# Kernel optimization log

Measured on AMD Instinct MI355X. Metric: run time of the kernel, lower is better.

Reference implementation:

```python
import jax, jax.numpy as jnp
import numpy as np

B, N, DIM = 1, 512, 1024
HEADS, DH = 16, 64          # dim_head = 64, _dim = heads*dh = 1024
P = 32                      # projection_dim
P2 = P // 2
NEG_INF = -1e30


def setup_inputs() -> dict:
    key = jax.random.key(0)
    ks = jax.random.split(key, 14)
    s = 0.02
    _dim = HEADS * DH
    return {
        "x":    jax.random.normal(ks[0], (B, N, DIM), dtype=jnp.float32),
        "Wqkv": jax.random.normal(ks[1], (3 * _dim, DIM), dtype=jnp.float32) * s,
        "Wout": jax.random.normal(ks[2], (DIM, _dim), dtype=jnp.float32) * s,
        "Wq":   jax.random.normal(ks[3], (P, DH), dtype=jnp.float32) * s,
        "bq":   jax.random.normal(ks[4], (P,), dtype=jnp.float32) * s,
        "Wk":   jax.random.normal(ks[5], (P, DH), dtype=jnp.float32) * s,
        "bk":   jax.random.normal(ks[6], (P,), dtype=jnp.float32) * s,
        "W1":   jax.random.normal(ks[7], (P, 2 * P), dtype=jnp.float32) * s,
        "b1":   jax.random.normal(ks[8], (P,), dtype=jnp.float32) * s,
        "W2":   jax.random.normal(ks[9], (P2, P), dtype=jnp.float32) * s,
        "b2":   jax.random.normal(ks[10], (P2,), dtype=jnp.float32) * s,
        "W3":   jax.random.normal(ks[11], (1, P2), dtype=jnp.float32) * s,
        "b3":   jax.random.normal(ks[12], (1,), dtype=jnp.float32) * s,
    }


def reference(x, Wqkv, Wout, Wq, bq, Wk, bk, W1, b1, W2, b2, W3, b3):
    b, n, _ = x.shape
    # qkv projection, then einops 'b n (d k h) -> k b h n d' split (d outermost!)
    qkv = jnp.einsum('bnc,oc->bno', x, Wqkv).reshape(b, n, DH, 3, HEADS)
    q = jnp.transpose(qkv[:, :, :, 0, :], (0, 3, 1, 2))  # [b,h,n,dh]
    k = jnp.transpose(qkv[:, :, :, 1, :], (0, 3, 1, 2))
    v = jnp.transpose(qkv[:, :, :, 2, :], (0, 3, 1, 2))

    qp = jnp.einsum('bhnd,pd->bhnp', q, Wq) + bq  # [b,h,n,P]
    kp = jnp.einsum('bhnd,pd->bhnp', k, Wk) + bk

    # linear1 on concat(q_i, k_j): split W1 -> broadcast-add (same math,
    # avoids materializing the [b,h,n,n,2P] concat tensor)
    W1q, W1k = W1[:, :P], W1[:, P:]
    a = jnp.einsum('bhnp,qp->bhnq', qp, W1q)      # [b,h,n,P]
    c = jnp.einsum('bhnp,qp->bhnq', kp, W1k)      # [b,h,n,P]
    h1 = jax.nn.relu(a[:, :, :, None, :] + c[:, :, None, :, :] + b1)  # [b,h,n,n,P]
    h2 = jax.nn.relu(jnp.einsum('bhijp,qp->bhijq', h1, W2) + b2)      # [b,h,n,n,P/2]
    score = jnp.einsum('bhijq,oq->bhijo', h2, W3)[..., 0] + b3[0]     # [b,h,n,n]

    # causal mask (triu(1) filled with -inf)
    i = jnp.arange(n)
    causal = i[None, :] > i[:, None]
    score = jnp.where(causal, NEG_INF, score)

    attn = jax.nn.softmax(score, axis=-1)
    out = jnp.einsum('bhij,bhjd->bhid', attn, v)                      # [b,h,n,dh]
    out = jnp.transpose(out, (0, 2, 1, 3)).reshape(b, n, HEADS * DH)  # b n (h d)
    return jnp.einsum('bne,oe->bno', out, Wout)
```

## Files before the change

### kernel.cpp

```cpp
#include <hip/hip_runtime.h>
#include <hip/hip_bf16.h>
#include <hip/hip_fp16.h>
#include <math.h>

#define N_SEQ 512
#define DIM   1024
#define HEADS 16
#define DH    64
#define P     32
#define P2    16
#define PSTR  520

typedef short    bf16x8 __attribute__((ext_vector_type(8)));
typedef _Float16 f16x8  __attribute__((ext_vector_type(8)));
typedef float    f32x4  __attribute__((ext_vector_type(4)));

__device__ inline unsigned short f2bf(float f) {
  union { float f; unsigned u; } v; v.f = f;
  unsigned r = (v.u + 0x7fffu + ((v.u >> 16) & 1u)) >> 16;
  return (unsigned short)r;
}

union H8 { f16x8 v; __half2 h2[4]; unsigned u32[4]; };

__global__ __launch_bounds__(256) void prep(
    const float* __restrict__ Wqkv, const float* __restrict__ Wq,
    const float* __restrict__ bq, const float* __restrict__ Wk,
    const float* __restrict__ bk, const float* __restrict__ W1,
    const float* __restrict__ x, const float* __restrict__ Wout,
    short* __restrict__ Wcomb, short* __restrict__ xb,
    short* __restrict__ Woutb, float* __restrict__ ba32,
    float* __restrict__ bc32) {
  const int b = blockIdx.x, tid = threadIdx.x;
  if (b < 256) {
    __shared__ float W1s[32][33];
    __shared__ float Wqs[32][65];
    __shared__ float wsm[32][65];
    __shared__ __align__(16) float qs[64][132];
    const int part = b >> 7, rem = b & 127;
    const int h = rem >> 3, c0 = (rem & 7) * 128;
    const int grow = part * 16 + h;
    for (int idx = tid; idx < 1024; idx += 256)
      W1s[idx >> 5][idx & 31] = W1[(idx >> 5) * 64 + part * 32 + (idx & 31)];
    const float* Wsel = part ? Wk : Wq;
    for (int idx = tid; idx < 2048; idx += 256)
      Wqs[idx >> 6][idx & 63] = Wsel[idx];
    for (int idx = tid; idx < 2048; idx += 256) {
      const int d = idx >> 5, c4 = idx & 31;
      *(float4*)&qs[d][c4 * 4] =
          *(const float4*)(Wqkv + (size_t)(d * 48 + grow) * DIM + c0 + c4 * 4);
    }
    __syncthreads();
    for (int idx = tid; idx < 2048; idx += 256) {
      const int q = idx >> 6, d = idx & 63;
      float s = 0.f;
#pragma unroll
      for (int p = 0; p < 32; ++p) s += W1s[q][p] * Wqs[p][d];
      wsm[q][d] = s;
    }
    __syncthreads();
    for (int idx = tid; idx < 4096; idx += 256) {
      const int q = idx >> 7, c = idx & 127;
      float s = 0.f;
#pragma unroll
      for (int d = 0; d < 64; ++d) s += wsm[q][d] * qs[d][c];
      Wcomb[(size_t)(part * 512 + h * 32 + q) * DIM + c0 + c] = (short)f2bf(s);
    }
    if (rem == 0 && tid < 32) {
      const float* bsel = part ? bk : bq;
      float s = 0.f;
#pragma unroll
      for (int p = 0; p < 32; ++p) s += W1s[tid][p] * bsel[p];
      (part ? bc32 : ba32)[tid] = s;
    }
  } else if (b < 384) {
#pragma unroll
    for (int rr = 0; rr < 8; ++rr) {
      const int ov = (b - 256) * 8 + rr;
      const int h = ov >> 6, d = ov & 63;
      const float4 v = *(const float4*)(Wqkv + (size_t)(d * 48 + 32 + h) * DIM + tid * 4);
      ushort4 o;
      o.x = f2bf(v.x); o.y = f2bf(v.y); o.z = f2bf(v.z); o.w = f2bf(v.w);
      *(ushort4*)(Wcomb + (size_t)(1024 + ov) * DIM + tid * 4) = o;
    }
  } else if (b < 512) {
    const int idx = (b - 384) * 256 + tid;
#pragma unroll
    for (int u = 0; u < 4; ++u) {
      const int t = u * 32768 + idx;
      const float4 v = ((const float4*)x)[t];
      ushort4 o;
      o.x = f2bf(v.x); o.y = f2bf(v.y); o.z = f2bf(v.z); o.w = f2bf(v.w);
      ((ushort4*)xb)[t] = o;
    }
  } else {
    const int idx = (b - 512) * 256 + tid;
#pragma unroll
    for (int u = 0; u < 4; ++u) {
      const int t = u * 65536 + idx;
      const float4 v = ((const float4*)Wout)[t];
      ushort4 o;
      o.x = f2bf(v.x); o.y = f2bf(v.y); o.z = f2bf(v.z); o.w = f2bf(v.w);
      ((ushort4*)Woutb)[t] = o;
    }
  }
}

__global__ __launch_bounds__(256) void gemm_acv(
    const short* __restrict__ xb, const short* __restrict__ Wcomb,
    const float* __restrict__ ba32, const float* __restrict__ bc32,
    const float* __restrict__ b1,
    __half* __restrict__ a_buf, __half* __restrict__ cb_buf,
    __half* __restrict__ vT) {
  const int wave = blockIdx.x * 4 + (threadIdx.x >> 6);
  const int tm = wave >> 6;
  const int tn = wave & 63;
  const int lane = threadIdx.x & 63;
  const int m = lane & 15;
  const int quad = lane >> 4;

  const short* pa  = xb + (size_t)(tm * 16 + m) * DIM + quad * 8;
  const short* pb0 = Wcomb + (size_t)(tn * 32 + m) * DIM + quad * 8;
  const short* pb1 = pb0 + (size_t)16 * DIM;

  f32x4 acc0 = {0.f,0.f,0.f,0.f}, acc1 = {0.f,0.f,0.f,0.f};
#pragma unroll 4
  for (int k = 0; k < DIM; k += 32) {
    const bf16x8 av = *(const bf16x8*)(pa + k);
    const bf16x8 b0 = *(const bf16x8*)(pb0 + k);
    const bf16x8 b1v = *(const bf16x8*)(pb1 + k);
    acc0 = __builtin_amdgcn_mfma_f32_16x16x32_bf16(av, b0, acc0, 0, 0, 0);
    acc1 = __builtin_amdgcn_mfma_f32_16x16x32_bf16(av, b1v, acc1, 0, 0, 0);
  }

#pragma unroll
  for (int r = 0; r < 4; ++r) {
    const int n = tm * 16 + quad * 4 + r;
#pragma unroll
    for (int half = 0; half < 2; ++half) {
      const int o = tn * 32 + m + half * 16;
      const float val = half ? acc1[r] : acc0[r];
      if (o < 512) {
        const int h = o >> 5, q = o & 31;
        a_buf[((size_t)h * N_SEQ + n) * P + q] = __float2half(val + ba32[q]);
      } else if (o < 1024) {
        const int oo = o - 512, h = oo >> 5, q = oo & 31;
        cb_buf[((size_t)h * N_SEQ + n) * P + q] = __float2half(val + bc32[q] + b1[q]);
      } else {
        const int ov = o - 1024, h = ov >> 6, d = ov & 63;
        vT[((size_t)h * DH + d) * N_SEQ + n] = __float2half(val);
      }
    }
  }
}

__device__ inline float rowscore(const H8& a, const H8& c, f16x8 w2f,
                                 float4 b2q, float4 w3q) {
  H8 u;
#pragma unroll
  for (int k = 0; k < 4; ++k) {
    const __half2 s = __hadd2(a.h2[k], c.h2[k]);
    union { __half2 h; unsigned u; } cv; cv.h = s;
    const unsigned msk = (cv.u >> 15) & 0x00010001u;
    u.u32[k] = cv.u & ~(msk * 0xFFFFu);
  }
  f32x4 acc = {0.f, 0.f, 0.f, 0.f};
  acc = __builtin_amdgcn_mfma_f32_16x16x32_f16(w2f, u.v, acc, 0, 0, 0);
  return fmaxf(acc[0] + b2q.x, 0.f) * w3q.x + fmaxf(acc[1] + b2q.y, 0.f) * w3q.y
       + fmaxf(acc[2] + b2q.z, 0.f) * w3q.z + fmaxf(acc[3] + b2q.w, 0.f) * w3q.w;
}

__device__ inline float quadreduce4(float p0, float p1, float p2, float p3,
                                    int quad) {
  const float sx = (quad & 1) ? p0 : p1;
  const float sy = (quad & 1) ? p2 : p3;
  const float rx = __shfl_xor(sx, 16);
  const float ry = __shfl_xor(sy, 16);
  const float aa = ((quad & 1) ? p1 : p0) + rx;
  const float bb = ((quad & 1) ? p3 : p2) + ry;
  const float sz = (quad & 2) ? aa : bb;
  const float rz = __shfl_xor(sz, 32);
  return ((quad & 2) ? bb : aa) + rz;
}

__global__ __launch_bounds__(256) void attn_fused(
    const __half* __restrict__ a_g, const __half* __restrict__ cb_g,
    const float* __restrict__ W2, const float* __restrict__ b2,
    const float* __restrict__ W3,
    const __half* __restrict__ vT, short* __restrict__ attnb) {
  const int p = blockIdx.x;
  const int h = blockIdx.y;
  const int tid = threadIdx.x;
  const int w = tid >> 6;
  const int lane = tid & 63;
  const int m = lane & 15, quad = lane >> 4;

  __shared__ __align__(16) __half probS[32][PSTR];
  __shared__ float invS[32];

  const int tlo = p, thi = 31 - p;
  const int nlo = p + 1, nhi = 32 - p;

  {
    f16x8 w2f;
    {
      const float4* wp = (const float4*)(W2 + m * P + quad * 8);
      const float4 w0 = wp[0], w1 = wp[1];
      H8 u;
      u.h2[0] = __floats2half2_rn(w0.x, w0.y);
      u.h2[1] = __floats2half2_rn(w0.z, w0.w);
      u.h2[2] = __floats2half2_rn(w1.x, w1.y);
      u.h2[3] = __floats2half2_rn(w1.z, w1.w);
      w2f = u.v;
    }
    const float4 b2q = *(const float4*)(b2 + quad * 4);
    const float4 w3q = *(const float4*)(W3 + quad * 4);

    H8 alo[4], ahi[4];
#pragma unroll
    for (int r = 0; r < 4; ++r) {
      alo[r].v = *(const f16x8*)(a_g + ((size_t)h * N_SEQ + tlo * 16 + 4 * w + r) * P + quad * 8);
      ahi[r].v = *(const f16x8*)(a_g + ((size_t)h * N_SEQ + thi * 16 + 4 * w + r) * P + quad * 8);
    }

    for (int jt = 0; jt < nhi; ++jt) {
      H8 cb;
      cb.v = *(const f16x8*)(cb_g + ((size_t)h * N_SEQ + jt * 16 + m) * P + quad * 8);
      const float q0 = rowscore(ahi[0], cb, w2f, b2q, w3q);
      const float q1 = rowscore(ahi[1], cb, w2f, b2q, w3q);
      const float q2 = rowscore(ahi[2], cb, w2f, b2q, w3q);
      const float q3 = rowscore(ahi[3], cb, w2f, b2q, w3q);
      const float fh = quadreduce4(q0, q1, q2, q3, quad);
      probS[16 + 4 * w + quad][jt * 16 + m] = __float2half(fh);
      if (jt < nlo) {
        const float s0 = rowscore(alo[0], cb, w2f, b2q, w3q);
        const float s1 = rowscore(alo[1], cb, w2f, b2q, w3q);
        const float s2 = rowscore(alo[2], cb, w2f, b2q, w3q);
        const float s3 = rowscore(alo[3], cb, w2f, b2q, w3q);
        const float fl = quadreduce4(s0, s1, s2, s3, quad);
        probS[4 * w + quad][jt * 16 + m] = __float2half(fl);
      }
    }
  }
  __syncthreads();

  {
    const int lr = 8 * w + (lane >> 3);
    const int c  = lane & 7;
    const int gi = (lr < 16) ? (tlo * 16 + lr) : (thi * 16 + (lr - 16));
    float mx = -1e30f;
#pragma unroll
    for (int k = 0; k < 8; ++k) {
      const int c0 = k * 64 + c * 8;
      if (c0 > gi) break;
      H8 vv; vv.v = *(const f16x8*)&probS[lr][c0];
#pragma unroll
      for (int u = 0; u < 8; ++u) {
        const float s = __half2float(vv.h2[u >> 1].data[u & 1]);
        if (c0 + u <= gi) mx = fmaxf(mx, s);
      }
    }
#pragma unroll
    for (int msk = 1; msk < 8; msk <<= 1) mx = fmaxf(mx, __shfl_xor(mx, msk));
    float sum = 0.f;
#pragma unroll
    for (int k = 0; k < 8; ++k) {
      const int c0 = k * 64 + c * 8;
      H8 vv; vv.v = *(const f16x8*)&probS[lr][c0];
      H8 o;
#pragma unroll
      for (int u = 0; u < 4; ++u) {
        float e0 = 0.f, e1 = 0.f;
        if (c0 + 2 * u <= gi) {
          e0 = __expf(__half2float(vv.h2[u].data[0]) - mx);
          if (c0 + 2 * u + 1 <= gi)
            e1 = __expf(__half2float(vv.h2[u].data[1]) - mx);
        }
        sum += e0 + e1;
        o.h2[u] = __floats2half2_rn(e0, e1);
      }
      *(f16x8*)&probS[lr][c0] = o.v;
    }
#pragma unroll
    for (int msk = 1; msk < 8; msk <<= 1) sum += __shfl_xor(sum, msk);
    if (c == 0) invS[lr] = 1.f / sum;
  }
  __syncthreads();

  {
    const int d0 = w * 16;
    const __half* pb = vT + ((size_t)h * DH + d0 + m) * N_SEQ + quad * 8;
#pragma unroll
    for (int half = 0; half < 2; ++half) {
      const int lbase = half ? 16 : 0;
      const int tile = half ? thi : tlo;
      const int nk = half ? ((33 - p) >> 1) : ((p + 2) >> 1);
      f32x4 acc = {0.f, 0.f, 0.f, 0.f};
      for (int k = 0; k < nk; ++k) {
        const f16x8 a = *(const f16x8*)&probS[lbase + m][k * 32 + quad * 8];
        const f16x8 b = *(const f16x8*)(pb + k * 32);
        acc = __builtin_amdgcn_mfma_f32_16x16x32_f16(a, b, acc, 0, 0, 0);
      }
#pragma unroll
      for (int r = 0; r < 4; ++r) {
        const int lrow = quad * 4 + r;
        const float val = acc[r] * invS[lbase + lrow];
        attnb[(size_t)(tile * 16 + lrow) * DIM + h * DH + d0 + m] = (short)f2bf(val);
      }
    }
  }
}

__global__ __launch_bounds__(256) void gemm_out16(
    const short* __restrict__ A, const short* __restrict__ B,
    float* __restrict__ C) {
  const int wave = blockIdx.x * 4 + (threadIdx.x >> 6);
  const int tm = wave >> 6;
  const int tn = wave & 63;
  const int lane = threadIdx.x & 63;
  const int m = lane & 15, quad = lane >> 4;

  const short* pa = A + (size_t)(tm * 16 + m) * DIM + quad * 8;
  const short* pb = B + (size_t)(tn * 16 + m) * DIM + quad * 8;

  f32x4 acc = {0.f, 0.f, 0.f, 0.f};
#pragma unroll 4
  for (int k = 0; k < DIM; k += 32) {
    const bf16x8 a = *(const bf16x8*)(pa + k);
    const bf16x8 b = *(const bf16x8*)(pb + k);
    acc = __builtin_amdgcn_mfma_f32_16x16x32_bf16(a, b, acc, 0, 0, 0);
  }
#pragma unroll
  for (int r = 0; r < 4; ++r)
    C[(size_t)(tm * 16 + quad * 4 + r) * DIM + tn * 16 + m] = acc[r];
}

extern "C" void kernel_launch(void* const* d_in, const int* in_sizes, int n_in,
                              void* d_out, int out_size, void* d_ws, size_t ws_size,
                              hipStream_t stream) {
  const float* x    = (const float*)d_in[0];
  const float* Wqkv = (const float*)d_in[1];
  const float* Wout = (const float*)d_in[2];
  const float* Wq   = (const float*)d_in[3];
  const float* bq   = (const float*)d_in[4];
  const float* Wk   = (const float*)d_in[5];
  const float* bk   = (const float*)d_in[6];
  const float* W1   = (const float*)d_in[7];
  const float* b1   = (const float*)d_in[8];
  const float* W2   = (const float*)d_in[9];
  const float* b2   = (const float*)d_in[10];
  const float* W3   = (const float*)d_in[11];
  float* out = (float*)d_out;

  float*  ws     = (float*)d_ws;
  float*  ba32   = ws;
  float*  bc32   = ba32 + 32;
  __half* a_buf  = (__half*)(bc32 + 32);
  __half* cb_buf = a_buf + (size_t)HEADS * N_SEQ * P;
  __half* vT     = cb_buf + (size_t)HEADS * N_SEQ * P;
  short*  Wcomb  = (short*)(vT + (size_t)HEADS * DH * N_SEQ);
  short*  xb     = Wcomb + (size_t)2048 * DIM;
  short*  Woutb  = xb + (size_t)N_SEQ * DIM;
  short*  attnb  = Woutb + (size_t)DIM * DIM;

  prep<<<768, 256, 0, stream>>>(Wqkv, Wq, bq, Wk, bk, W1, x, Wout,
                                Wcomb, xb, Woutb, ba32, bc32);

  gemm_acv<<<512, 256, 0, stream>>>(xb, Wcomb, ba32, bc32, b1,
                                    a_buf, cb_buf, vT);

  dim3 g3(16, HEADS);
  attn_fused<<<g3, 256, 0, stream>>>(a_buf, cb_buf, W2, b2, W3, vT, attnb);

  gemm_out16<<<512, 256, 0, stream>>>(attnb, Woutb, out);
}
```

Baseline: 174.1 us.

## Fuse all four stages into one cooperative persistent kernel with grid syncs

Replaces the four separate launches (prep, qkv-projection GEMM, fused attention, output GEMM) with a single cooperative kernel of 256 blocks that runs each stage as a phase separated by grid-wide synchronisation. The GEMM phases now loop twice per wave and the prep work is redistributed across the 256 blocks, with shared memory carved from one static buffer. The aim is to remove inter-kernel launch gaps and tail effects. In exchange, the GEMM phases run with half as many resident waves, which reduces latency hiding, and each phase boundary adds grid-sync cost. A non-cooperative four-launch fallback is kept.

```diff
diff --git a/kernel.cpp b/kernel.cpp
--- a/kernel.cpp
+++ b/kernel.cpp
@@ -1,15 +1,19 @@
 #include <hip/hip_runtime.h>
+#include <hip/hip_cooperative_groups.h>
 #include <hip/hip_bf16.h>
 #include <hip/hip_fp16.h>
 #include <math.h>
+
+namespace cg = cooperative_groups;
 
 #define N_SEQ 512
 #define DIM   1024
 #define HEADS 16
 #define DH    64
 #define P     32
-#define P2    16
 #define PSTR  520
+
+#define SMEM_BYTES 54656
 
 typedef short    bf16x8 __attribute__((ext_vector_type(8)));
 typedef _Float16 f16x8  __attribute__((ext_vector_type(8)));
@@ -22,137 +26,6 @@
 }
 
 union H8 { f16x8 v; __half2 h2[4]; unsigned u32[4]; };
-
-__global__ __launch_bounds__(256) void prep(
-    const float* __restrict__ Wqkv, const float* __restrict__ Wq,
-    const float* __restrict__ bq, const float* __restrict__ Wk,
-    const float* __restrict__ bk, const float* __restrict__ W1,
-    const float* __restrict__ x, const float* __restrict__ Wout,
-    short* __restrict__ Wcomb, short* __restrict__ xb,
-    short* __restrict__ Woutb, float* __restrict__ ba32,
-    float* __restrict__ bc32) {
-  const int b = blockIdx.x, tid = threadIdx.x;
-  if (b < 256) {
-    __shared__ float W1s[32][33];
-    __shared__ float Wqs[32][65];
-    __shared__ float wsm[32][65];
-    __shared__ __align__(16) float qs[64][132];
-    const int part = b >> 7, rem = b & 127;
-    const int h = rem >> 3, c0 = (rem & 7) * 128;
-    const int grow = part * 16 + h;
-    for (int idx = tid; idx < 1024; idx += 256)
-      W1s[idx >> 5][idx & 31] = W1[(idx >> 5) * 64 + part * 32 + (idx & 31)];
-    const float* Wsel = part ? Wk : Wq;
-    for (int idx = tid; idx < 2048; idx += 256)
-      Wqs[idx >> 6][idx & 63] = Wsel[idx];
-    for (int idx = tid; idx < 2048; idx += 256) {
-      const int d = idx >> 5, c4 = idx & 31;
-      *(float4*)&qs[d][c4 * 4] =
-          *(const float4*)(Wqkv + (size_t)(d * 48 + grow) * DIM + c0 + c4 * 4);
-    }
-    __syncthreads();
-    for (int idx = tid; idx < 2048; idx += 256) {
-      const int q = idx >> 6, d = idx & 63;
-      float s = 0.f;
-#pragma unroll
-      for (int p = 0; p < 32; ++p) s += W1s[q][p] * Wqs[p][d];
-      wsm[q][d] = s;
-    }
-    __syncthreads();
-    for (int idx = tid; idx < 4096; idx += 256) {
-      const int q = idx >> 7, c = idx & 127;
-      float s = 0.f;
-#pragma unroll
-      for (int d = 0; d < 64; ++d) s += wsm[q][d] * qs[d][c];
-      Wcomb[(size_t)(part * 512 + h * 32 + q) * DIM + c0 + c] = (short)f2bf(s);
-    }
-    if (rem == 0 && tid < 32) {
-      const float* bsel = part ? bk : bq;
-      float s = 0.f;
-#pragma unroll
-      for (int p = 0; p < 32; ++p) s += W1s[tid][p] * bsel[p];
-      (part ? bc32 : ba32)[tid] = s;
-    }
-  } else if (b < 384) {
-#pragma unroll
-    for (int rr = 0; rr < 8; ++rr) {
-      const int ov = (b - 256) * 8 + rr;
-      const int h = ov >> 6, d = ov & 63;
-      const float4 v = *(const float4*)(Wqkv + (size_t)(d * 48 + 32 + h) * DIM + tid * 4);
-      ushort4 o;
-      o.x = f2bf(v.x); o.y = f2bf(v.y); o.z = f2bf(v.z); o.w = f2bf(v.w);
-      *(ushort4*)(Wcomb + (size_t)(1024 + ov) * DIM + tid * 4) = o;
-    }
-  } else if (b < 512) {
-    const int idx = (b - 384) * 256 + tid;
-#pragma unroll
-    for (int u = 0; u < 4; ++u) {
-      const int t = u * 32768 + idx;
-      const float4 v = ((const float4*)x)[t];
-      ushort4 o;
-      o.x = f2bf(v.x); o.y = f2bf(v.y); o.z = f2bf(v.z); o.w = f2bf(v.w);
-      ((ushort4*)xb)[t] = o;
-    }
-  } else {
-    const int idx = (b - 512) * 256 + tid;
-#pragma unroll
-    for (int u = 0; u < 4; ++u) {
-      const int t = u * 65536 + idx;
-      const float4 v = ((const float4*)Wout)[t];
-      ushort4 o;
-      o.x = f2bf(v.x); o.y = f2bf(v.y); o.z = f2bf(v.z); o.w = f2bf(v.w);
-      ((ushort4*)Woutb)[t] = o;
-    }
-  }
-}
-
-__global__ __launch_bounds__(256) void gemm_acv(
-    const short* __restrict__ xb, const short* __restrict__ Wcomb,
-    const float* __restrict__ ba32, const float* __restrict__ bc32,
-    const float* __restrict__ b1,
-    __half* __restrict__ a_buf, __half* __restrict__ cb_buf,
-    __half* __restrict__ vT) {
-  const int wave = blockIdx.x * 4 + (threadIdx.x >> 6);
-  const int tm = wave >> 6;
-  const int tn = wave & 63;
-  const int lane = threadIdx.x & 63;
-  const int m = lane & 15;
-  const int quad = lane >> 4;
-
-  const short* pa  = xb + (size_t)(tm * 16 + m) * DIM + quad * 8;
-  const short* pb0 = Wcomb + (size_t)(tn * 32 + m) * DIM + quad * 8;
-  const short* pb1 = pb0 + (size_t)16 * DIM;
-
-  f32x4 acc0 = {0.f,0.f,0.f,0.f}, acc1 = {0.f,0.f,0.f,0.f};
-#pragma unroll 4
-  for (int k = 0; k < DIM; k += 32) {
-    const bf16x8 av = *(const bf16x8*)(pa + k);
-    const bf16x8 b0 = *(const bf16x8*)(pb0 + k);
-    const bf16x8 b1v = *(const bf16x8*)(pb1 + k);
-    acc0 = __builtin_amdgcn_mfma_f32_16x16x32_bf16(av, b0, acc0, 0, 0, 0);
-    acc1 = __builtin_amdgcn_mfma_f32_16x16x32_bf16(av, b1v, acc1, 0, 0, 0);
-  }
-
-#pragma unroll
-  for (int r = 0; r < 4; ++r) {
-    const int n = tm * 16 + quad * 4 + r;
-#pragma unroll
-    for (int half = 0; half < 2; ++half) {
-      const int o = tn * 32 + m + half * 16;
-      const float val = half ? acc1[r] : acc0[r];
-      if (o < 512) {
-        const int h = o >> 5, q = o & 31;
-        a_buf[((size_t)h * N_SEQ + n) * P + q] = __float2half(val + ba32[q]);
-      } else if (o < 1024) {
-        const int oo = o - 512, h = oo >> 5, q = oo & 31;
-        cb_buf[((size_t)h * N_SEQ + n) * P + q] = __float2half(val + bc32[q] + b1[q]);
-      } else {
-        const int ov = o - 1024, h = ov >> 6, d = ov & 63;
-        vT[((size_t)h * DH + d) * N_SEQ + n] = __float2half(val);
-      }
-    }
-  }
-}
 
 __device__ inline float rowscore(const H8& a, const H8& c, f16x8 w2f,
                                  float4 b2q, float4 w3q) {
@@ -183,20 +56,153 @@
   return ((quad & 2) ? bb : aa) + rz;
 }
 
-__global__ __launch_bounds__(256) void attn_fused(
-    const __half* __restrict__ a_g, const __half* __restrict__ cb_g,
-    const float* __restrict__ W2, const float* __restrict__ b2,
-    const float* __restrict__ W3,
-    const __half* __restrict__ vT, short* __restrict__ attnb) {
-  const int p = blockIdx.x;
-  const int h = blockIdx.y;
-  const int tid = threadIdx.x;
+__device__ void phase_prep(int bx, int tid, char* smem,
+                           const float* Wqkv, const float* Wq, const float* bq,
+                           const float* Wk, const float* bk, const float* W1,
+                           const float* x, const float* Wout,
+                           short* Wcomb, short* xb, short* Woutb,
+                           float* ba32, float* bc32) {
+  float* W1s = (float*)smem;
+  float* Wqs = W1s + 32 * 33;
+  float* wsm = Wqs + 32 * 65;
+  float* qs  = wsm + 32 * 65;
+
+  const int part = bx >> 7, rem = bx & 127;
+  const int h = rem >> 3, c0 = (rem & 7) * 128;
+  const int grow = part * 16 + h;
+  for (int idx = tid; idx < 1024; idx += 256)
+    W1s[(idx >> 5) * 33 + (idx & 31)] =
+        W1[(idx >> 5) * 64 + part * 32 + (idx & 31)];
+  const float* Wsel = part ? Wk : Wq;
+  for (int idx = tid; idx < 2048; idx += 256)
+    Wqs[(idx >> 6) * 65 + (idx & 63)] = Wsel[idx];
+  for (int idx = tid; idx < 2048; idx += 256) {
+    const int d = idx >> 5, c4 = idx & 31;
+    *(float4*)&qs[d * 132 + c4 * 4] =
+        *(const float4*)(Wqkv + (size_t)(d * 48 + grow) * DIM + c0 + c4 * 4);
+  }
+  __syncthreads();
+  for (int idx = tid; idx < 2048; idx += 256) {
+    const int q = idx >> 6, d = idx & 63;
+    float s = 0.f;
+#pragma unroll
+    for (int p = 0; p < 32; ++p) s += W1s[q * 33 + p] * Wqs[p * 65 + d];
+    wsm[q * 65 + d] = s;
+  }
+  __syncthreads();
+  for (int idx = tid; idx < 4096; idx += 256) {
+    const int q = idx >> 7, c = idx & 127;
+    float s = 0.f;
+#pragma unroll
+    for (int d = 0; d < 64; ++d) s += wsm[q * 65 + d] * qs[d * 132 + c];
+    Wcomb[(size_t)(part * 512 + h * 32 + q) * DIM + c0 + c] = (short)f2bf(s);
+  }
+  if (rem == 0 && tid < 32) {
+    const float* bsel = part ? bk : bq;
+    float s = 0.f;
+#pragma unroll
+    for (int p = 0; p < 32; ++p) s += W1s[tid * 33 + p] * bsel[p];
+    (part ? bc32 : ba32)[tid] = s;
+  }
+
+#pragma unroll
+  for (int rr = 0; rr < 4; ++rr) {
+    const int ov = bx * 4 + rr;
+    const int vh = ov >> 6, vd = ov & 63;
+    const float4 v = *(const float4*)(Wqkv + (size_t)(vd * 48 + 32 + vh) * DIM + tid * 4);
+    ushort4 o;
+    o.x = f2bf(v.x); o.y = f2bf(v.y); o.z = f2bf(v.z); o.w = f2bf(v.w);
+    *(ushort4*)(Wcomb + (size_t)(1024 + ov) * DIM + tid * 4) = o;
+  }
+  {
+    const int idx = bx * 256 + tid;
+#pragma unroll
+    for (int u = 0; u < 2; ++u) {
+      const int t = u * 65536 + idx;
+      const float4 v = ((const float4*)x)[t];
+      ushort4 o;
+      o.x = f2bf(v.x); o.y = f2bf(v.y); o.z = f2bf(v.z); o.w = f2bf(v.w);
+      ((ushort4*)xb)[t] = o;
+    }
+  }
+  {
+    const int idx = bx * 256 + tid;
+#pragma unroll
+    for (int u = 0; u < 4; ++u) {
+      const int t = u * 65536 + idx;
+      const float4 v = ((const float4*)Wout)[t];
+      ushort4 o;
+      o.x = f2bf(v.x); o.y = f2bf(v.y); o.z = f2bf(v.z); o.w = f2bf(v.w);
+      ((ushort4*)Woutb)[t] = o;
+    }
+  }
+}
+
+__device__ void phase_acv(int bx, int tid,
+                          const short* xb, const short* Wcomb,
+                          const float* ba32, const float* bc32,
+                          const float* b1,
+                          __half* a_buf, __half* cb_buf, __half* vT) {
+  const int wave0 = bx * 4 + (tid >> 6);
+  const int lane = tid & 63;
+  const int m = lane & 15;
+  const int quad = lane >> 4;
+
+#pragma unroll
+  for (int rep = 0; rep < 2; ++rep) {
+    const int wv = wave0 + rep * 1024;
+    const int tm = wv >> 6;
+    const int tn = wv & 63;
+
+    const short* pa  = xb + (size_t)(tm * 16 + m) * DIM + quad * 8;
+    const short* pb0 = Wcomb + (size_t)(tn * 32 + m) * DIM + quad * 8;
+    const short* pb1 = pb0 + (size_t)16 * DIM;
+
+    f32x4 acc0 = {0.f,0.f,0.f,0.f}, acc1 = {0.f,0.f,0.f,0.f};
+#pragma unroll 4
+    for (int k = 0; k < DIM; k += 32) {
+      const bf16x8 av = *(const bf16x8*)(pa + k);
+      const bf16x8 b0 = *(const bf16x8*)(pb0 + k);
+      const bf16x8 b1v = *(const bf16x8*)(pb1 + k);
+      acc0 = __builtin_amdgcn_mfma_f32_16x16x32_bf16(av, b0, acc0, 0, 0, 0);
+      acc1 = __builtin_amdgcn_mfma_f32_16x16x32_bf16(av, b1v, acc1, 0, 0, 0);
+    }
+
+#pragma unroll
+    for (int r = 0; r < 4; ++r) {
+      const int n = tm * 16 + quad * 4 + r;
+#pragma unroll
+      for (int half = 0; half < 2; ++half) {
+        const int o = tn * 32 + m + half * 16;
+        const float val = half ? acc1[r] : acc0[r];
+        if (o < 512) {
+          const int h = o >> 5, q = o & 31;
+          a_buf[((size_t)h * N_SEQ + n) * P + q] = __float2half(val + ba32[q]);
+        } else if (o < 1024) {
+          const int oo = o - 512, h = oo >> 5, q = oo & 31;
+          cb_buf[((size_t)h * N_SEQ + n) * P + q] =
+              __float2half(val + bc32[q] + b1[q]);
+        } else {
+          const int ov = o - 1024, h = ov >> 6, d = ov & 63;
+          vT[((size_t)h * DH + d) * N_SEQ + n] = __float2half(val);
+        }
+      }
+    }
+  }
+}
+
+__device__ void phase_attn(int bx, int tid, char* smem,
+                           const __half* a_buf, const __half* cb_buf,
+                           const float* W2, const float* b2, const float* W3,
+                           const __half* vT, short* attnb) {
+  __half* probS = (__half*)smem;
+  float* invS = (float*)(smem + 32 * PSTR * 2);
+
+  const int p = bx & 15;
+  const int h = bx >> 4;
   const int w = tid >> 6;
   const int lane = tid & 63;
   const int m = lane & 15, quad = lane >> 4;
-
-  __shared__ __align__(16) __half probS[32][PSTR];
-  __shared__ float invS[32];
 
   const int tlo = p, thi = 31 - p;
   const int nlo = p + 1, nhi = 32 - p;
@@ -219,26 +225,26 @@
     H8 alo[4], ahi[4];
 #pragma unroll
     for (int r = 0; r < 4; ++r) {
-      alo[r].v = *(const f16x8*)(a_g + ((size_t)h * N_SEQ + tlo * 16 + 4 * w + r) * P + quad * 8);
-      ahi[r].v = *(const f16x8*)(a_g + ((size_t)h * N_SEQ + thi * 16 + 4 * w + r) * P + quad * 8);
+      alo[r].v = *(const f16x8*)(a_buf + ((size_t)h * N_SEQ + tlo * 16 + 4 * w + r) * P + quad * 8);
+      ahi[r].v = *(const f16x8*)(a_buf + ((size_t)h * N_SEQ + thi * 16 + 4 * w + r) * P + quad * 8);
     }
 
     for (int jt = 0; jt < nhi; ++jt) {
       H8 cb;
-      cb.v = *(const f16x8*)(cb_g + ((size_t)h * N_SEQ + jt * 16 + m) * P + quad * 8);
+      cb.v = *(const f16x8*)(cb_buf + ((size_t)h * N_SEQ + jt * 16 + m) * P + quad * 8);
       const float q0 = rowscore(ahi[0], cb, w2f, b2q, w3q);
       const float q1 = rowscore(ahi[1], cb, w2f, b2q, w3q);
       const float q2 = rowscore(ahi[2], cb, w2f, b2q, w3q);
       const float q3 = rowscore(ahi[3], cb, w2f, b2q, w3q);
       const float fh = quadreduce4(q0, q1, q2, q3, quad);
-      probS[16 + 4 * w + quad][jt * 16 + m] = __float2half(fh);
+      probS[(16 + 4 * w + quad) * PSTR + jt * 16 + m] = __float2half(fh);
       if (jt < nlo) {
         const float s0 = rowscore(alo[0], cb, w2f, b2q, w3q);
         const float s1 = rowscore(alo[1], cb, w2f, b2q, w3q);
         const float s2 = rowscore(alo[2], cb, w2f, b2q, w3q);
         const float s3 = rowscore(alo[3], cb, w2f, b2q, w3q);
         const float fl = quadreduce4(s0, s1, s2, s3, quad);
-        probS[4 * w + quad][jt * 16 + m] = __float2half(fl);
+        probS[(4 * w + quad) * PSTR + jt * 16 + m] = __float2half(fl);
       }
     }
   }
@@ -253,7 +259,7 @@
     for (int k = 0; k < 8; ++k) {
       const int c0 = k * 64 + c * 8;
       if (c0 > gi) break;
-      H8 vv; vv.v = *(const f16x8*)&probS[lr][c0];
+      H8 vv; vv.v = *(const f16x8*)&probS[lr * PSTR + c0];
 #pragma unroll
       for (int u = 0; u < 8; ++u) {
         const float s = __half2float(vv.h2[u >> 1].data[u & 1]);
@@ -266,7 +272,7 @@
 #pragma unroll
     for (int k = 0; k < 8; ++k) {
       const int c0 = k * 64 + c * 8;
-      H8 vv; vv.v = *(const f16x8*)&probS[lr][c0];
+      H8 vv; vv.v = *(const f16x8*)&probS[lr * PSTR + c0];
       H8 o;
 #pragma unroll
       for (int u = 0; u < 4; ++u) {
@@ -279,7 +285,7 @@
         sum += e0 + e1;
         o.h2[u] = __floats2half2_rn(e0, e1);
       }
-      *(f16x8*)&probS[lr][c0] = o.v;
+      *(f16x8*)&probS[lr * PSTR + c0] = o.v;
     }
 #pragma unroll
     for (int msk = 1; msk < 8; msk <<= 1) sum += __shfl_xor(sum, msk);
@@ -297,7 +303,7 @@
       const int nk = half ? ((33 - p) >> 1) : ((p + 2) >> 1);
       f32x4 acc = {0.f, 0.f, 0.f, 0.f};
       for (int k = 0; k < nk; ++k) {
-        const f16x8 a = *(const f16x8*)&probS[lbase + m][k * 32 + quad * 8];
+        const f16x8 a = *(const f16x8*)&probS[(lbase + m) * PSTR + k * 32 + quad * 8];
         const f16x8 b = *(const f16x8*)(pb + k * 32);
         acc = __builtin_amdgcn_mfma_f32_16x16x32_f16(a, b, acc, 0, 0, 0);
       }
@@ -305,34 +311,99 @@
       for (int r = 0; r < 4; ++r) {
         const int lrow = quad * 4 + r;
         const float val = acc[r] * invS[lbase + lrow];
-        attnb[(size_t)(tile * 16 + lrow) * DIM + h * DH + d0 + m] = (short)f2bf(val);
-      }
-    }
-  }
-}
-
-__global__ __launch_bounds__(256) void gemm_out16(
-    const short* __restrict__ A, const short* __restrict__ B,
-    float* __restrict__ C) {
-  const int wave = blockIdx.x * 4 + (threadIdx.x >> 6);
-  const int tm = wave >> 6;
-  const int tn = wave & 63;
-  const int lane = threadIdx.x & 63;
+        attnb[(size_t)(tile * 16 + lrow) * DIM + h * DH + d0 + m] =
+            (short)f2bf(val);
+      }
+    }
+  }
+}
+
+__device__ void phase_out(int bx, int tid, const short* attnb,
+                          const short* Woutb, float* out) {
+  const int wave0 = bx * 4 + (tid >> 6);
+  const int lane = tid & 63;
   const int m = lane & 15, quad = lane >> 4;
 
-  const short* pa = A + (size_t)(tm * 16 + m) * DIM + quad * 8;
-  const short* pb = B + (size_t)(tn * 16 + m) * DIM + quad * 8;
-
-  f32x4 acc = {0.f, 0.f, 0.f, 0.f};
+#pragma unroll
+  for (int rep = 0; rep < 2; ++rep) {
+    const int wv = wave0 + rep * 1024;
+    const int tm = wv >> 6;
+    const int tn = wv & 63;
+
+    const short* pa = attnb + (size_t)(tm * 16 + m) * DIM + quad * 8;
+    const short* pb = Woutb + (size_t)(tn * 16 + m) * DIM + quad * 8;
+
+    f32x4 acc = {0.f, 0.f, 0.f, 0.f};
 #pragma unroll 4
-  for (int k = 0; k < DIM; k += 32) {
-    const bf16x8 a = *(const bf16x8*)(pa + k);
-    const bf16x8 b = *(const bf16x8*)(pb + k);
-    acc = __builtin_amdgcn_mfma_f32_16x16x32_bf16(a, b, acc, 0, 0, 0);
-  }
-#pragma unroll
-  for (int r = 0; r < 4; ++r)
-    C[(size_t)(tm * 16 + quad * 4 + r) * DIM + tn * 16 + m] = acc[r];
+    for (int k = 0; k < DIM; k += 32) {
+      const bf16x8 a = *(const bf16x8*)(pa + k);
+      const bf16x8 b = *(const bf16x8*)(pb + k);
+      acc = __builtin_amdgcn_mfma_f32_16x16x32_bf16(a, b, acc, 0, 0, 0);
+    }
+#pragma unroll
+    for (int r = 0; r < 4; ++r)
+      out[(size_t)(tm * 16 + quad * 4 + r) * DIM + tn * 16 + m] = acc[r];
+  }
+}
+
+__global__ __launch_bounds__(256) void fused_all(
+    const float* __restrict__ Wqkv, const float* __restrict__ Wq,
+    const float* __restrict__ bq, const float* __restrict__ Wk,
+    const float* __restrict__ bk, const float* __restrict__ W1,
+    const float* __restrict__ x, const float* __restrict__ Wout,
+    const float* __restrict__ b1, const float* __restrict__ W2,
+    const float* __restrict__ b2, const float* __restrict__ W3,
+    short* __restrict__ Wcomb, short* __restrict__ xb,
+    short* __restrict__ Woutb, float* __restrict__ ba32,
+    float* __restrict__ bc32, __half* __restrict__ a_buf,
+    __half* __restrict__ cb_buf, __half* __restrict__ vT,
+    short* __restrict__ attnb, float* __restrict__ out) {
+  cg::grid_group grid = cg::this_grid();
+  const int bx = blockIdx.x;
+  const int tid = threadIdx.x;
+  __shared__ __align__(16) char smem[SMEM_BYTES];
+
+  phase_prep(bx, tid, smem, Wqkv, Wq, bq, Wk, bk, W1, x, Wout,
+             Wcomb, xb, Woutb, ba32, bc32);
+  __threadfence();
+  grid.sync();
+
+  phase_acv(bx, tid, xb, Wcomb, ba32, bc32, b1, a_buf, cb_buf, vT);
+  __threadfence();
+  grid.sync();
+
+  __syncthreads();
+  phase_attn(bx, tid, smem, a_buf, cb_buf, W2, b2, W3, vT, attnb);
+  __threadfence();
+  grid.sync();
+
+  phase_out(bx, tid, attnb, Woutb, out);
+}
+
+__global__ __launch_bounds__(256) void k_prep(
+    const float* Wqkv, const float* Wq, const float* bq, const float* Wk,
+    const float* bk, const float* W1, const float* x, const float* Wout,
+    short* Wcomb, short* xb, short* Woutb, float* ba32, float* bc32) {
+  __shared__ __align__(16) char smem[SMEM_BYTES];
+  phase_prep(blockIdx.x, threadIdx.x, smem, Wqkv, Wq, bq, Wk, bk, W1, x, Wout,
+             Wcomb, xb, Woutb, ba32, bc32);
+}
+__global__ __launch_bounds__(256) void k_acv(
+    const short* xb, const short* Wcomb, const float* ba32, const float* bc32,
+    const float* b1, __half* a_buf, __half* cb_buf, __half* vT) {
+  phase_acv(blockIdx.x, threadIdx.x, xb, Wcomb, ba32, bc32, b1,
+            a_buf, cb_buf, vT);
+}
+__global__ __launch_bounds__(256) void k_attn(
+    const __half* a_buf, const __half* cb_buf, const float* W2,
+    const float* b2, const float* W3, const __half* vT, short* attnb) {
+  __shared__ __align__(16) char smem[SMEM_BYTES];
+  phase_attn(blockIdx.x, threadIdx.x, smem, a_buf, cb_buf, W2, b2, W3, vT,
+             attnb);
+}
+__global__ __launch_bounds__(256) void k_out(
+    const short* attnb, const short* Woutb, float* out) {
+  phase_out(blockIdx.x, threadIdx.x, attnb, Woutb, out);
 }
 
 extern "C" void kernel_launch(void* const* d_in, const int* in_sizes, int n_in,
@@ -363,14 +434,17 @@
   short*  Woutb  = xb + (size_t)N_SEQ * DIM;
   short*  attnb  = Woutb + (size_t)DIM * DIM;
 
-  prep<<<768, 256, 0, stream>>>(Wqkv, Wq, bq, Wk, bk, W1, x, Wout,
-                                Wcomb, xb, Woutb, ba32, bc32);
-
-  gemm_acv<<<512, 256, 0, stream>>>(xb, Wcomb, ba32, bc32, b1,
-                                    a_buf, cb_buf, vT);
-
-  dim3 g3(16, HEADS);
-  attn_fused<<<g3, 256, 0, stream>>>(a_buf, cb_buf, W2, b2, W3, vT, attnb);
-
-  gemm_out16<<<512, 256, 0, stream>>>(attnb, Woutb, out);
-}
+  void* args[] = {&Wqkv, &Wq, &bq, &Wk, &bk, &W1, &x, &Wout, &b1, &W2, &b2,
+                  &W3, &Wcomb, &xb, &Woutb, &ba32, &bc32, &a_buf, &cb_buf,
+                  &vT, &attnb, &out};
+  hipError_t e = hipLaunchCooperativeKernel((void*)fused_all, dim3(256),
+                                            dim3(256), args, 0, stream);
+  if (e != hipSuccess) {
+    k_prep<<<256, 256, 0, stream>>>(Wqkv, Wq, bq, Wk, bk, W1, x, Wout,
+                                    Wcomb, xb, Woutb, ba32, bc32);
+    k_acv<<<256, 256, 0, stream>>>(xb, Wcomb, ba32, bc32, b1,
+                                   a_buf, cb_buf, vT);
+    k_attn<<<256, 256, 0, stream>>>(a_buf, cb_buf, W2, b2, W3, vT, attnb);
+    k_out<<<256, 256, 0, stream>>>(attnb, Woutb, out);
+  }
+}
```

Result: slower. 394.9 us (+126.8%).
